# Performance work log

Measured on AMD Instinct MI355X. Metric: run time of the kernel, lower is better.

Reference implementation:

```python
import jax, jax.numpy as jnp
import numpy as np

THR = 0.5      # span-selection threshold
K_SUBJ = 16    # max subject/object spans kept per sentence (padded)
K_OBJ = 8      # max object spans kept per (subject, relation)

# Greedy threshold-based span pairing: for each start position i with
# start_prob>THR, take the first unused j>=i with end_prob>THR (NMS-like).
# Returns fixed-size padded spans [K,2] (int32) and a validity mask [K].
def greedy_spans(sp, ep, K):
    S = sp.shape[0]
    idxs = jnp.arange(S, dtype=jnp.int32)
    def step(carry, i):
        used, count, spans, valid = carry
        gate = sp[i] > THR
        cand = (ep > THR) & (~used) & (idxs >= i)
        has = jnp.any(cand)
        j = jnp.argmax(cand).astype(jnp.int32)  # first True
        found = gate & has
        slot = jnp.minimum(count, K - 1)
        write = found & (count < K)
        pair = jnp.where(write, jnp.stack([i, j]).astype(jnp.int32), spans[slot])
        spans = spans.at[slot].set(pair)
        valid = valid.at[slot].set(valid[slot] | write)
        used = used.at[j].set(used[j] | found)
        count = count + found.astype(jnp.int32)
        return (used, count, spans, valid), None
    init = (jnp.zeros(S, bool), jnp.int32(0),
            jnp.zeros((K, 2), jnp.int32), jnp.zeros(K, bool))
    (_, _, spans, valid), _ = jax.lax.scan(step, init, idxs)
    return spans, valid


def _model(token_embs, hg, rel_embs, b_rel_transe, head_w, head_b,
           Wmats, Wbias, rproj_w, rproj_b, V_w, V_b):
    # head_w/head_b order: 0 start_subj, 1 end_subj, 2 b_start_obj, 3 b_end_obj,
    #                      4 start_obj, 5 end_obj, 6 b_start_subj, 7 b_end_subj
    # Wmats/Wbias order:   0 W_s, 1 W_r, 2 W_g, 3 W_x, 4 W_r_b, 5 W_g_b, 6 W_x_b, 7 W_x2
    sig = jax.nn.sigmoid
    head = lambda x, i: sig(x @ head_w[i] + head_b[i])        # H->1 sigmoid head
    lin = lambda x, i: x @ Wmats[i].T + Wbias[i]              # H->H linear

    # ---- first-level span scores + greedy extraction (forward & backward) ----
    sub_sp, sub_ep = head(token_embs, 0), head(token_embs, 1)   # [B,S]
    bob_sp, bob_ep = head(token_embs, 2), head(token_embs, 3)
    g = jax.vmap(lambda a, b: greedy_spans(a, b, K_SUBJ))
    subj_spans, subj_valid = g(sub_sp, sub_ep)                  # [B,K,2],[B,K]
    b_subj_spans, b_subj_valid = g(bob_sp, bob_ep)

    def gather(tok_b, spans, valid):  # mean of start/end token embeddings
        e = (tok_b[spans[:, 0]] + tok_b[spans[:, 1]]) * 0.5
        return e * valid[:, None].astype(tok_b.dtype)
    s_k = jax.vmap(gather)(token_embs, subj_spans, subj_valid)      # [B,K,H]
    b_s_k = jax.vmap(gather)(token_embs, b_subj_spans, b_subj_valid)
    s_k_w = lin(s_k, 0) * subj_valid[..., None]                     # W_s + mask
    b_s_k_w = lin(b_s_k, 0) * b_subj_valid[..., None]

    # ---- relation-aware attention context C = sum_s A[b,s,r] * x[b,s] ----
    b_rel = b_rel_transe @ rproj_w.T + rproj_b                      # r_proj
    def attend(rels, ir, ig, ix):
        e = jnp.tanh(lin(token_embs, ix)[:, :, None, :]             # [B,S,1,H]
                     + lin(hg, ig)[:, None, None, :]                # [B,1,1,H]
                     + lin(rels, ir)[None, None, :, :])             # [1,1,R,H]
        v = e @ V_w + V_b[0]                                        # [B,S,R]
        A = jax.nn.softmax(v, axis=1)                               # over seq
        return jnp.einsum('bsr,bsh->brh', A, token_embs)            # [B,R,H]
    C = attend(rel_embs, 1, 2, 3)
    b_C = attend(b_rel, 4, 5, 6)

    # Heads are linear, so distribute w over the sum instead of
    # materializing the [B,S,K,R,H] tensor.
    tok_mix = token_embs + lin(token_embs, 7)
    def pair_probs(Cmat, skw, i):
        t_tok = tok_mix @ head_w[i]                                 # [B,S]
        t_sub = skw @ head_w[i]                                     # [B,K]
        t_rel = Cmat @ head_w[i]                                    # [B,R]
        return sig(t_tok[:, :, None, None] + t_sub[:, None, :, None]
                   + t_rel[:, None, None, :] + head_b[i])           # [B,S,K,R]
    obj_sp, obj_ep = pair_probs(C, s_k_w, 4), pair_probs(C, s_k_w, 5)
    bsub_sp, bsub_ep = pair_probs(b_C, b_s_k_w, 6), pair_probs(b_C, b_s_k_w, 7)

    # ---- greedy object-span extraction per (batch, subject, relation) ----
    def triples(sp4, ep4, subj_ok):
        B_, S_, K_, R_ = sp4.shape
        fsp = sp4.transpose(0, 2, 3, 1).reshape(-1, S_)
        fep = ep4.transpose(0, 2, 3, 1).reshape(-1, S_)
        spans, valid = jax.vmap(lambda a, b: greedy_spans(a, b, K_OBJ))(fsp, fep)
        spans = spans.reshape(B_, K_, R_, K_OBJ, 2)
        valid = valid.reshape(B_, K_, R_, K_OBJ) & subj_ok[:, :, None, None]
        return spans, valid
    f_spans, f_valid = triples(obj_sp, obj_ep, subj_valid)
    bw_spans, bw_valid = triples(bsub_sp, bsub_ep, b_subj_valid)

    probs = jnp.stack([obj_sp, obj_ep, bsub_sp, bsub_ep])           # [4,B,S,K,R]
    return (probs, subj_spans, subj_valid, b_subj_spans, b_subj_valid,
            f_spans, f_valid, bw_spans, bw_valid)


def setup_inputs() -> dict:
    key = jax.random.key(0)
    ks = jax.random.split(key, 12)
    B, S, H, R, T = 8, 256, 768, 40, 80
    sc = H ** -0.5
    return {
        'token_embs': jax.random.normal(ks[0], (B, S, H), jnp.float32),
        'hg': jax.random.normal(ks[1], (B, H), jnp.float32),
        'rel_embs': jax.random.normal(ks[2], (R, H), jnp.float32),
        'b_rel_transe': jax.random.normal(ks[3], (R, T), jnp.float32),
        'head_w': jax.random.normal(ks[4], (8, H), jnp.float32) * sc,
        'head_b': jax.random.normal(ks[5], (8,), jnp.float32) * 0.1,
        'Wmats': jax.random.normal(ks[6], (8, H, H), jnp.float32) * sc,
        'Wbias': jax.random.normal(ks[7], (8, H), jnp.float32) * 0.02,
        'rproj_w': jax.random.normal(ks[8], (H, T), jnp.float32) * (T ** -0.5),
        'rproj_b': jax.random.normal(ks[9], (H,), jnp.float32) * 0.02,
        'V_w': jax.random.normal(ks[10], (H,), jnp.float32) * sc,
        'V_b': jax.random.normal(ks[11], (1,), jnp.float32) * 0.1,
    }


def reference(token_embs, hg, rel_embs, b_rel_transe, head_w, head_b,
              Wmats, Wbias, rproj_w, rproj_b, V_w, V_b):
    return _model(token_embs, hg, rel_embs, b_rel_transe, head_w, head_b,
                  Wmats, Wbias, rproj_w, rproj_b, V_w, V_b)
```

## Files before the change

kernel.cpp:

```cpp
#include <hip/hip_runtime.h>
#include <hip/hip_bf16.h>
#include <stdint.h>

#define Bc 8
#define Sc 256
#define Hc 768
#define Rc 40
#define Tc 80
#define KSc 16
#define KOc 8

#define OUT_SSP 5242880
#define OUT_SVA 5243136
#define OUT_BSP 5243264
#define OUT_BVA 5243520
#define OUT_FSP 5243648
#define OUT_FVA 5325568
#define OUT_WSP 5366528
#define OUT_WVA 5448448

#define CM_PS (16 * Rc * Hc)

__device__ inline double wave_reduce_d(double v) {
#pragma unroll
  for (int o = 32; o; o >>= 1) v += __shfl_down(v, o, 64);
  return v;
}
__device__ inline float wave_reduce_f(float v) {
#pragma unroll
  for (int o = 32; o; o >>= 1) v += __shfl_down(v, o, 64);
  return v;
}

__device__ inline float tanh_fast(float x) {
  float t = __builtin_amdgcn_exp2f(x * 2.8853900817779268f);
  return fmaf(-2.f, __builtin_amdgcn_rcpf(t + 1.f), 1.f);
}

__global__ __launch_bounds__(256) void k_l03(const float* __restrict__ x,
                                             const float* __restrict__ head_w,
                                             const float* __restrict__ head_b,
                                             float* __restrict__ l03) {
  int bs = blockIdx.x * 4 + (threadIdx.x >> 6);
  int lane = threadIdx.x & 63;
  if (bs >= Bc * Sc) return;
  const float* xr = x + (size_t)bs * Hc;
  double acc[4] = {0.0, 0.0, 0.0, 0.0};
  for (int h = lane; h < Hc; h += 64) {
    double xv = (double)xr[h];
    acc[0] += xv * (double)head_w[h];
    acc[1] += xv * (double)head_w[Hc + h];
    acc[2] += xv * (double)head_w[2 * Hc + h];
    acc[3] += xv * (double)head_w[3 * Hc + h];
  }
#pragma unroll
  for (int i = 0; i < 4; ++i) {
    double a = wave_reduce_d(acc[i]);
    if (lane == 0) l03[i * (Bc * Sc) + bs] = (float)(a + (double)head_b[i]);
  }
}

__device__ inline int find_first(const uint64_t* epm, const uint64_t* used, int i) {
  int wi = i >> 6;
  uint64_t m = epm[wi] & ~used[wi] & (~0ull << (i & 63));
  if (m) return (wi << 6) + (__ffsll((unsigned long long)m) - 1);
  for (int w = wi + 1; w < 4; ++w) {
    uint64_t mm = epm[w] & ~used[w];
    if (mm) return (w << 6) + (__ffsll((unsigned long long)mm) - 1);
  }
  return -1;
}

__global__ __launch_bounds__(64) void k_greedy1(const float* __restrict__ l03,
                                                int* __restrict__ spans1, int* __restrict__ valid1,
                                                float* __restrict__ out) {
  int t = blockIdx.x;
  int dir = t >> 3, b = t & 7;
  int lane = threadIdx.x;
  const float* sp = l03 + (dir * 2) * (Bc * Sc) + b * Sc;
  const float* ep = sp + Bc * Sc;
  uint64_t spm[4], epm[4];
#pragma unroll
  for (int w = 0; w < 4; ++w) {
    spm[w] = __ballot(sp[w * 64 + lane] > 0.f);
    epm[w] = __ballot(ep[w * 64 + lane] > 0.f);
  }
  __shared__ int ssp0[KSc], ssp1[KSc], sva[KSc];
  if (lane < KSc) { ssp0[lane] = 0; ssp1[lane] = 0; sva[lane] = 0; }
  __syncthreads();
  if (lane == 0) {
    uint64_t used[4] = {0, 0, 0, 0};
    int cnt = 0;
#pragma unroll
    for (int w = 0; w < 4; ++w) {
      uint64_t g = spm[w];
      while (g) {
        int bit = __ffsll((unsigned long long)g) - 1;
        g &= g - 1;
        int i = w * 64 + bit;
        int j = find_first(epm, used, i);
        if (j < 0) continue;
        used[j >> 6] |= (1ull << (j & 63));
        if (cnt < KSc) { ssp0[cnt] = i; ssp1[cnt] = j; sva[cnt] = 1; }
        cnt++;
      }
    }
  }
  __syncthreads();
  int base = (dir * Bc + b) * KSc;
  float* osp = out + (dir ? OUT_BSP : OUT_SSP) + b * KSc * 2;
  float* ova = out + (dir ? OUT_BVA : OUT_SVA) + b * KSc;
  if (lane < KSc) {
    spans1[(base + lane) * 2] = ssp0[lane];
    spans1[(base + lane) * 2 + 1] = ssp1[lane];
    valid1[base + lane] = sva[lane];
    osp[lane * 2] = (float)ssp0[lane];
    osp[lane * 2 + 1] = (float)ssp1[lane];
    ova[lane] = (float)sva[lane];
  }
}

__global__ __launch_bounds__(256) void k_brel(const float* __restrict__ brt,
                                              const float* __restrict__ rw,
                                              const float* __restrict__ rb,
                                              float* __restrict__ brel) {
  int idx = blockIdx.x * blockDim.x + threadIdx.x;
  if (idx >= Rc * Hc) return;
  int r = idx / Hc, h = idx % Hc;
  float acc = rb[h];
  const float* a = brt + r * Tc;
  const float* w = rw + (size_t)h * Tc;
  for (int t = 0; t < Tc; ++t) acc = fmaf(a[t], w[t], acc);
  brel[idx] = acc;
}

__global__ __launch_bounds__(256) void k_egather(const float* __restrict__ x,
                                                 const int* __restrict__ spans1,
                                                 float* __restrict__ eb) {
  int row = blockIdx.x;
  int b = (row / KSc) % Bc;
  int s0 = spans1[row * 2], s1 = spans1[row * 2 + 1];
  const float* x0 = x + ((size_t)b * Sc + s0) * Hc;
  const float* x1 = x + ((size_t)b * Sc + s1) * Hc;
  float* er = eb + (size_t)row * Hc;
  for (int h = threadIdx.x; h < Hc; h += 256) er[h] = 0.5f * (x0[h] + x1[h]);
}

__global__ __launch_bounds__(256) void k_skw(const float* __restrict__ eb,
                                             const float* __restrict__ Wmats,
                                             const float* __restrict__ Wbias,
                                             const int* __restrict__ valid1,
                                             float* __restrict__ skw) {
  int m0 = blockIdx.y * 32;
  int n0 = blockIdx.x * 64;
  __shared__ float Asl[32][36];
  __shared__ float Bsl[32][68];
  int tid = threadIdx.x;
  int arow = tid >> 3, acol = (tid & 7) << 2;
  int brow = tid >> 2, bcol = (tid & 3) << 2;
  int txi = tid & 15, tyi = tid >> 4;
  const float* ap = eb + (size_t)(m0 + arow) * Hc + acol;
  const float* bp = Wmats + (size_t)(n0 + brow) * Hc + bcol;
  int nb = n0 + txi * 4;
  float4 bias = *(const float4*)&Wbias[nb];
  float acc[2][4];
#pragma unroll
  for (int i = 0; i < 2; ++i) { acc[i][0] = bias.x; acc[i][1] = bias.y; acc[i][2] = bias.z; acc[i][3] = bias.w; }
  for (int k0 = 0; k0 < Hc; k0 += 32) {
    float4 av = *(const float4*)(ap + k0);
    float4 b0 = *(const float4*)(bp + k0);
    float4 b1 = *(const float4*)(bp + k0 + 16);
    __syncthreads();
    Asl[acol + 0][arow] = av.x; Asl[acol + 1][arow] = av.y; Asl[acol + 2][arow] = av.z; Asl[acol + 3][arow] = av.w;
    Bsl[bcol + 0][brow] = b0.x; Bsl[bcol + 1][brow] = b0.y; Bsl[bcol + 2][brow] = b0.z; Bsl[bcol + 3][brow] = b0.w;
    Bsl[bcol + 16][brow] = b1.x; Bsl[bcol + 17][brow] = b1.y; Bsl[bcol + 18][brow] = b1.z; Bsl[bcol + 19][brow] = b1.w;
    __syncthreads();
#pragma unroll
    for (int kk = 0; kk < 32; ++kk) {
      float a0 = Asl[kk][tyi * 2], a1 = Asl[kk][tyi * 2 + 1];
      float4 b = *(const float4*)&Bsl[kk][txi * 4];
      acc[0][0] = fmaf(a0, b.x, acc[0][0]); acc[0][1] = fmaf(a0, b.y, acc[0][1]);
      acc[0][2] = fmaf(a0, b.z, acc[0][2]); acc[0][3] = fmaf(a0, b.w, acc[0][3]);
      acc[1][0] = fmaf(a1, b.x, acc[1][0]); acc[1][1] = fmaf(a1, b.y, acc[1][1]);
      acc[1][2] = fmaf(a1, b.z, acc[1][2]); acc[1][3] = fmaf(a1, b.w, acc[1][3]);
    }
  }
  int m_ = m0 + tyi * 2;
#pragma unroll
  for (int i = 0; i < 2; ++i) {
    int v = valid1[m_ + i];
    float4 o;
    o.x = v ? acc[i][0] : 0.f; o.y = v ? acc[i][1] : 0.f;
    o.z = v ? acc[i][2] : 0.f; o.w = v ? acc[i][3] : 0.f;
    *(float4*)&skw[(size_t)(m_ + i) * Hc + nb] = o;
  }
}

__global__ __launch_bounds__(256) void k_tgtr(const float* __restrict__ hg,
                                              const float* __restrict__ rel,
                                              const float* __restrict__ brel,
                                              const float* __restrict__ Wmats,
                                              const float* __restrict__ Wbias,
                                              float* __restrict__ tg,
                                              float* __restrict__ tr) {
  int grp = blockIdx.z;
  const float* Asrc; int M; int wsel; float* dst;
  if (grp == 0)      { Asrc = hg;   M = 8;  wsel = 2; dst = tg; }
  else if (grp == 1) { Asrc = hg;   M = 8;  wsel = 5; dst = tg + 8 * Hc; }
  else if (grp == 2) { Asrc = rel;  M = 40; wsel = 1; dst = tr; }
  else               { Asrc = brel; M = 40; wsel = 4; dst = tr + 40 * Hc; }
  int m0 = blockIdx.y * 32;
  if (m0 >= M) return;
  int n0 = blockIdx.x * 64;
  const float* W = Wmats + (size_t)wsel * Hc * Hc;
  const float* bias = Wbias + wsel * Hc;
  __shared__ float Asl[32][36];
  __shared__ float Bsl[32][68];
  int tid = threadIdx.x;
  int arow = tid >> 3, acol = (tid & 7) << 2;
  int brow = tid >> 2, bcol = (tid & 3) << 2;
  int txi = tid & 15, tyi = tid >> 4;
  int ar = m0 + arow;
  const float* ap = Asrc + (size_t)(ar < M ? ar : 0) * Hc + acol;
  const float* bp = W + (size_t)(n0 + brow) * Hc + bcol;
  int nb = n0 + txi * 4;
  float4 bv = *(const float4*)&bias[nb];
  float acc[2][4];
#pragma unroll
  for (int i = 0; i < 2; ++i) { acc[i][0] = bv.x; acc[i][1] = bv.y; acc[i][2] = bv.z; acc[i][3] = bv.w; }
  for (int k0 = 0; k0 < Hc; k0 += 32) {
    float4 av = *(const float4*)(ap + k0);
    float4 b0 = *(const float4*)(bp + k0);
    float4 b1 = *(const float4*)(bp + k0 + 16);
    __syncthreads();
    Asl[acol + 0][arow] = av.x; Asl[acol + 1][arow] = av.y; Asl[acol + 2][arow] = av.z; Asl[acol + 3][arow] = av.w;
    Bsl[bcol + 0][brow] = b0.x; Bsl[bcol + 1][brow] = b0.y; Bsl[bcol + 2][brow] = b0.z; Bsl[bcol + 3][brow] = b0.w;
    Bsl[bcol + 16][brow] = b1.x; Bsl[bcol + 17][brow] = b1.y; Bsl[bcol + 18][brow] = b1.z; Bsl[bcol + 19][brow] = b1.w;
    __syncthreads();
#pragma unroll
    for (int kk = 0; kk < 32; ++kk) {
      float a0 = Asl[kk][tyi * 2], a1 = Asl[kk][tyi * 2 + 1];
      float4 b = *(const float4*)&Bsl[kk][txi * 4];
      acc[0][0] = fmaf(a0, b.x, acc[0][0]); acc[0][1] = fmaf(a0, b.y, acc[0][1]);
      acc[0][2] = fmaf(a0, b.z, acc[0][2]); acc[0][3] = fmaf(a0, b.w, acc[0][3]);
      acc[1][0] = fmaf(a1, b.x, acc[1][0]); acc[1][1] = fmaf(a1, b.y, acc[1][1]);
      acc[1][2] = fmaf(a1, b.z, acc[1][2]); acc[1][3] = fmaf(a1, b.w, acc[1][3]);
    }
  }
  int m_ = m0 + tyi * 2;
#pragma unroll
  for (int i = 0; i < 2; ++i) {
    if (m_ + i < M) {
      float4 o; o.x = acc[i][0]; o.y = acc[i][1]; o.z = acc[i][2]; o.w = acc[i][3];
      *(float4*)&dst[(size_t)(m_ + i) * Hc + nb] = o;
    }
  }
}

#define BM 64
#define BN 64
#define BKK 32
#define LDP 68
__global__ __launch_bounds__(256) void k_tx(const float* __restrict__ x,
                                            const float* __restrict__ Wmats,
                                            const float* __restrict__ Wbias,
                                            float* __restrict__ txo) {
  int dir = blockIdx.z;
  const float* W = Wmats + (size_t)(dir ? 6 : 3) * Hc * Hc;
  const float* bias = Wbias + (dir ? 6 : 3) * Hc;
  float* outp = txo + (size_t)dir * (Bc * Sc * Hc);
  int m0 = blockIdx.y * BM;
  int n0 = blockIdx.x * BN;
  __shared__ float Asl[BKK][LDP];
  __shared__ float Bsl[BKK][LDP];
  int tid = threadIdx.x;
  int lr = tid >> 2;
  int lc = (tid & 3) << 2;
  int txi = tid & 15, tyi = tid >> 4;
  const float* xp = x + (size_t)(m0 + lr) * Hc + lc;
  const float* wp = W + (size_t)(n0 + lr) * Hc + lc;
  float4 a0 = *(const float4*)(xp);
  float4 a1 = *(const float4*)(xp + 16);
  float4 b0 = *(const float4*)(wp);
  float4 b1 = *(const float4*)(wp + 16);
  float acc[4][4] = {};
  for (int k0 = 0; k0 < Hc; k0 += BKK) {
    __syncthreads();
    Asl[lc + 0][lr] = a0.x; Asl[lc + 1][lr] = a0.y; Asl[lc + 2][lr] = a0.z; Asl[lc + 3][lr] = a0.w;
    Asl[lc + 16][lr] = a1.x; Asl[lc + 17][lr] = a1.y; Asl[lc + 18][lr] = a1.z; Asl[lc + 19][lr] = a1.w;
    Bsl[lc + 0][lr] = b0.x; Bsl[lc + 1][lr] = b0.y; Bsl[lc + 2][lr] = b0.z; Bsl[lc + 3][lr] = b0.w;
    Bsl[lc + 16][lr] = b1.x; Bsl[lc + 17][lr] = b1.y; Bsl[lc + 18][lr] = b1.z; Bsl[lc + 19][lr] = b1.w;
    __syncthreads();
    if (k0 + BKK < Hc) {
      a0 = *(const float4*)(xp + k0 + BKK);
      a1 = *(const float4*)(xp + k0 + BKK + 16);
      b0 = *(const float4*)(wp + k0 + BKK);
      b1 = *(const float4*)(wp + k0 + BKK + 16);
    }
#pragma unroll
    for (int kk = 0; kk < BKK; ++kk) {
      float4 a = *(const float4*)&Asl[kk][tyi * 4];
      float4 b = *(const float4*)&Bsl[kk][txi * 4];
      acc[0][0] = fmaf(a.x, b.x, acc[0][0]); acc[0][1] = fmaf(a.x, b.y, acc[0][1]);
      acc[0][2] = fmaf(a.x, b.z, acc[0][2]); acc[0][3] = fmaf(a.x, b.w, acc[0][3]);
      acc[1][0] = fmaf(a.y, b.x, acc[1][0]); acc[1][1] = fmaf(a.y, b.y, acc[1][1]);
      acc[1][2] = fmaf(a.y, b.z, acc[1][2]); acc[1][3] = fmaf(a.y, b.w, acc[1][3]);
      acc[2][0] = fmaf(a.z, b.x, acc[2][0]); acc[2][1] = fmaf(a.z, b.y, acc[2][1]);
      acc[2][2] = fmaf(a.z, b.z, acc[2][2]); acc[2][3] = fmaf(a.z, b.w, acc[2][3]);
      acc[3][0] = fmaf(a.w, b.x, acc[3][0]); acc[3][1] = fmaf(a.w, b.y, acc[3][1]);
      acc[3][2] = fmaf(a.w, b.z, acc[3][2]); acc[3][3] = fmaf(a.w, b.w, acc[3][3]);
    }
  }
  int nb = n0 + txi * 4;
  float4 bb = *(const float4*)&bias[nb];
#pragma unroll
  for (int i2 = 0; i2 < 4; ++i2) {
    float4 o;
    o.x = acc[i2][0] + bb.x; o.y = acc[i2][1] + bb.y;
    o.z = acc[i2][2] + bb.z; o.w = acc[i2][3] + bb.w;
    *(float4*)&outp[(size_t)(m0 + tyi * 4 + i2) * Hc + nb] = o;
  }
}

__global__ __launch_bounds__(256) void k_v(const float* __restrict__ txo,
                                           const float* __restrict__ tg,
                                           const float* __restrict__ tr,
                                           const float* __restrict__ Vw,
                                           const float* __restrict__ Vb,
                                           float* __restrict__ va) {
  int id = blockIdx.x;
  int dir = id >> 9;
  int bs0 = (id & 511) * 4;
  int b = bs0 >> 8;
  int tid = threadIdx.x;
  int wv = tid >> 6, lane = tid & 63;
  const float* tgr = tg + (dir * Bc + b) * Hc;
  float xt[4][12], vw[12];
#pragma unroll
  for (int u = 0; u < 12; ++u) {
    int h = lane + 64 * u;
    vw[u] = Vw[h];
    float tgv = tgr[h];
#pragma unroll
    for (int si = 0; si < 4; ++si)
      xt[si][u] = txo[((size_t)dir * (Bc * Sc) + bs0 + si) * Hc + h] + tgv;
  }
  float vb0 = Vb[0];
  for (int q = 0; q < 10; ++q) {
    int r = wv * 10 + q;
    const float* trr = tr + ((size_t)dir * Rc + r) * Hc + lane;
    float p0 = 0.f, p1 = 0.f, p2 = 0.f, p3 = 0.f;
#pragma unroll
    for (int u = 0; u < 12; ++u) {
      float t = trr[64 * u];
      p0 = fmaf(tanh_fast(xt[0][u] + t), vw[u], p0);
      p1 = fmaf(tanh_fast(xt[1][u] + t), vw[u], p1);
      p2 = fmaf(tanh_fast(xt[2][u] + t), vw[u], p2);
      p3 = fmaf(tanh_fast(xt[3][u] + t), vw[u], p3);
    }
    p0 = wave_reduce_f(p0); p1 = wave_reduce_f(p1);
    p2 = wave_reduce_f(p2); p3 = wave_reduce_f(p3);
    if (lane == 0) {
      size_t base = ((size_t)dir * (Bc * Sc) + bs0) * Rc + r;
      va[base] = p0 + vb0;
      va[base + Rc] = p1 + vb0;
      va[base + 2 * Rc] = p2 + vb0;
      va[base + 3 * Rc] = p3 + vb0;
    }
  }
}

__global__ __launch_bounds__(256) void k_softmax(float* __restrict__ va) {
  int id = blockIdx.x;
  int dir = id / (Bc * Rc); int rem = id % (Bc * Rc);
  int b = rem / Rc; int r = rem % Rc;
  int s = threadIdx.x;
  float* base = va + (((size_t)dir * Bc + b) * Sc) * Rc + r;
  float v = base[(size_t)s * Rc];
  __shared__ float red[8];
  float m = v;
#pragma unroll
  for (int o = 32; o; o >>= 1) m = fmaxf(m, __shfl_xor(m, o, 64));
  if ((s & 63) == 0) red[s >> 6] = m;
  __syncthreads();
  if (s == 0) red[4] = fmaxf(fmaxf(red[0], red[1]), fmaxf(red[2], red[3]));
  __syncthreads();
  m = red[4];
  float e = expf(v - m);
  float t = e;
#pragma unroll
  for (int o = 32; o; o >>= 1) t += __shfl_xor(t, o, 64);
  __syncthreads();
  if ((s & 63) == 0) red[s >> 6] = t;
  __syncthreads();
  if (s == 0) red[4] = red[0] + red[1] + red[2] + red[3];
  __syncthreads();
  base[(size_t)s * Rc] = e / red[4];
}

__global__ __launch_bounds__(256, 1) void k_C(const float* __restrict__ va,
                                              const float* __restrict__ x,
                                              float* __restrict__ Cm4) {
  int id = blockIdx.x;
  int p = id & 3;
  int g = id >> 2;
  int b = g & 7;
  __shared__ float As_[64 * Rc];
  int tid = threadIdx.x;
  const float* vab = va + ((size_t)g * Sc + p * 64) * Rc;
  for (int idx = tid; idx < 64 * Rc; idx += 256) As_[idx] = vab[idx];
  __syncthreads();
  const float* xb = x + ((size_t)b * Sc + p * 64) * Hc;
  float acc[3][Rc];
#pragma unroll
  for (int j = 0; j < 3; ++j)
#pragma unroll
    for (int r = 0; r < Rc; ++r) acc[j][r] = 0.f;
  for (int s = 0; s < 64; ++s) {
    float xv0 = xb[(size_t)s * Hc + tid];
    float xv1 = xb[(size_t)s * Hc + 256 + tid];
    float xv2 = xb[(size_t)s * Hc + 512 + tid];
#pragma unroll
    for (int q = 0; q < 10; ++q) {
      float4 a4 = *(const float4*)&As_[s * Rc + q * 4];
      acc[0][q * 4 + 0] = fmaf(a4.x, xv0, acc[0][q * 4 + 0]);
      acc[0][q * 4 + 1] = fmaf(a4.y, xv0, acc[0][q * 4 + 1]);
      acc[0][q * 4 + 2] = fmaf(a4.z, xv0, acc[0][q * 4 + 2]);
      acc[0][q * 4 + 3] = fmaf(a4.w, xv0, acc[0][q * 4 + 3]);
      acc[1][q * 4 + 0] = fmaf(a4.x, xv1, acc[1][q * 4 + 0]);
      acc[1][q * 4 + 1] = fmaf(a4.y, xv1, acc[1][q * 4 + 1]);
      acc[1][q * 4 + 2] = fmaf(a4.z, xv1, acc[1][q * 4 + 2]);
      acc[1][q * 4 + 3] = fmaf(a4.w, xv1, acc[1][q * 4 + 3]);
      acc[2][q * 4 + 0] = fmaf(a4.x, xv2, acc[2][q * 4 + 0]);
      acc[2][q * 4 + 1] = fmaf(a4.y, xv2, acc[2][q * 4 + 1]);
      acc[2][q * 4 + 2] = fmaf(a4.z, xv2, acc[2][q * 4 + 2]);
      acc[2][q * 4 + 3] = fmaf(a4.w, xv2, acc[2][q * 4 + 3]);
    }
  }
#pragma unroll
  for (int r = 0; r < Rc; ++r) {
    size_t base = ((size_t)(p * 16 + g) * Rc + r) * Hc + tid;
    Cm4[base] = acc[0][r];
    Cm4[base + 256] = acc[1][r];
    Cm4[base + 512] = acc[2][r];
  }
}

__global__ __launch_bounds__(256) void k_hv(const float* __restrict__ Wmats,
                                            const float* __restrict__ head_w,
                                            double* __restrict__ hv) {
  int idx = blockIdx.x * blockDim.x + threadIdx.x;
  if (idx >= 4 * Hc) return;
  int i = idx / Hc, j = idx % Hc;
  const float* h4 = head_w + (4 + i) * Hc;
  const float* W7 = Wmats + (size_t)7 * Hc * Hc;
  double acc = (double)h4[j];
  for (int hh = 0; hh < Hc; ++hh)
    acc += (double)W7[(size_t)hh * Hc + j] * (double)h4[hh];
  hv[idx] = acc;
}

__global__ __launch_bounds__(256) void k_tt(const float* __restrict__ x,
                                            const double* __restrict__ hv,
                                            double* __restrict__ tt) {
  int bs = blockIdx.x * 4 + (threadIdx.x >> 6);
  int lane = threadIdx.x & 63;
  if (bs >= Bc * Sc) return;
  const float* xr = x + (size_t)bs * Hc;
  double acc[4] = {0.0, 0.0, 0.0, 0.0};
  for (int h = lane; h < Hc; h += 64) {
    double xv = (double)xr[h];
    acc[0] += xv * hv[h];
    acc[1] += xv * hv[Hc + h];
    acc[2] += xv * hv[2 * Hc + h];
    acc[3] += xv * hv[3 * Hc + h];
  }
#pragma unroll
  for (int i = 0; i < 4; ++i) {
    double a = wave_reduce_d(acc[i]);
    if (lane == 0) tt[i * (Bc * Sc) + bs] = a;
  }
}

__global__ __launch_bounds__(256) void k_tsc(const float* __restrict__ skw,
                                             const float* __restrict__ Cm4,
                                             const float* __restrict__ head_w,
                                             const float* __restrict__ Wbias,
                                             double* __restrict__ ts,
                                             double* __restrict__ trl,
                                             double* __restrict__ c4) {
  int wave = blockIdx.x * 4 + (threadIdx.x >> 6);
  int lane = threadIdx.x & 63;
  const float* src; const float* w; double* dst;
  bool partial4 = false;
  if (wave < 512) {
    int p = wave >> 7, rem = wave & 127;
    int b = rem >> 4, k = rem & 15, dir = p >> 1;
    src = skw + (((size_t)(dir * Bc + b)) * KSc + k) * Hc;
    w = head_w + (4 + p) * Hc;
    dst = ts + (p * Bc + b) * KSc + k;
  } else if (wave < 1792) {
    int q = wave - 512;
    int p = q / 320, rem = q % 320;
    int b = rem / Rc, r = rem % Rc, dir = p >> 1;
    src = Cm4 + ((size_t)(dir * Bc + b) * Rc + r) * Hc;
    w = head_w + (4 + p) * Hc;
    dst = trl + (p * Bc + b) * Rc + r;
    partial4 = true;
  } else if (wave < 1796) {
    int p = wave - 1792;
    src = Wbias + 7 * Hc;
    w = head_w + (4 + p) * Hc;
    dst = c4 + p;
  } else return;
  double acc = 0.0;
  if (partial4) {
    for (int h = lane; h < Hc; h += 64) {
      double cs = (double)src[h] + (double)src[h + CM_PS] +
                  (double)src[h + 2 * CM_PS] + (double)src[h + 3 * CM_PS];
      acc += cs * (double)w[h];
    }
  } else {
    for (int h = lane; h < Hc; h += 64) acc += (double)src[h] * (double)w[h];
  }
  acc = wave_reduce_d(acc);
  if (lane == 0) *dst = acc;
}

__global__ __launch_bounds__(256) void k_probs(const double* __restrict__ tt,
                                               const double* __restrict__ ts,
                                               const double* __restrict__ trl,
                                               const double* __restrict__ c4,
                                               const float* __restrict__ head_b,
                                               float* __restrict__ out) {
  int id = blockIdx.x;
  int b = id >> 8, s = id & 255;
  (void)s;
  __shared__ double tsb[4][KSc];
  __shared__ double trb[4][Rc];
  __shared__ double basep[4];
  int tid = threadIdx.x;
  if (tid < 64) { int p = tid >> 4, k = tid & 15; tsb[p][k] = ts[(p * Bc + b) * KSc + k]; }
  if (tid < 160) { int p = tid / Rc, r = tid % Rc; trb[p][r] = trl[(p * Bc + b) * Rc + r]; }
  if (tid < 4) basep[tid] = tt[tid * (Bc * Sc) + id] + c4[tid] + (double)head_b[4 + tid];
  __syncthreads();
#pragma unroll
  for (int p = 0; p < 4; ++p) {
    double base = basep[p];
    float* op = out + ((size_t)(p * Bc) * Sc + id) * (KSc * Rc);
    for (int kr = tid; kr < KSc * Rc; kr += 256) {
      int k = kr / Rc, r = kr - k * Rc;
      double l = base + tsb[p][k] + trb[p][r];
      op[kr] = 1.f / (1.f + expf(-(float)l));
    }
  }
}

__global__ __launch_bounds__(256) void k_greedy2(const double* __restrict__ tt,
                                                 const double* __restrict__ ts,
                                                 const double* __restrict__ trl,
                                                 const double* __restrict__ c4,
                                                 const float* __restrict__ head_b,
                                                 const int* __restrict__ valid1,
                                                 float* __restrict__ out) {
  int gid = blockIdx.x * blockDim.x + threadIdx.x;
  if (gid >= 2 * Bc * KSc * Rc) return;
  int dir = gid / (Bc * KSc * Rc);
  int rem = gid % (Bc * KSc * Rc);
  int b = rem / (KSc * Rc);
  int kr = rem % (KSc * Rc);
  int k = kr / Rc, r = kr % Rc;
  int p0 = dir * 2, p1 = p0 + 1;
  double off0 = ts[(p0 * Bc + b) * KSc + k] + trl[(p0 * Bc + b) * Rc + r] + c4[p0] + (double)head_b[4 + p0];
  double off1 = ts[(p1 * Bc + b) * KSc + k] + trl[(p1 * Bc + b) * Rc + r] + c4[p1] + (double)head_b[4 + p1];
  const double* t0 = tt + p0 * (Bc * Sc) + b * Sc;
  const double* t1 = tt + p1 * (Bc * Sc) + b * Sc;
  uint64_t spm[4], epm[4], used[4] = {0, 0, 0, 0};
#pragma unroll
  for (int w = 0; w < 4; ++w) {
    uint64_t ms = 0, me = 0;
    for (int bit = 0; bit < 64; ++bit) {
      int s = w * 64 + bit;
      if (t0[s] + off0 > 0.0) ms |= (1ull << bit);
      if (t1[s] + off1 > 0.0) me |= (1ull << bit);
    }
    spm[w] = ms; epm[w] = me;
  }
  float* osp = out + (dir ? OUT_WSP : OUT_FSP) + (size_t)rem * KOc * 2;
  float* ova = out + (dir ? OUT_WVA : OUT_FVA) + (size_t)rem * KOc;
  for (int o = 0; o < KOc; ++o) { osp[o * 2] = 0.f; osp[o * 2 + 1] = 0.f; ova[o] = 0.f; }
  float sval = valid1[(dir * Bc + b) * KSc + k] ? 1.f : 0.f;
  int cnt = 0;
  for (int w = 0; w < 4; ++w) {
    uint64_t g = spm[w];
    while (g) {
      int bit = __ffsll((unsigned long long)g) - 1;
      g &= g - 1;
      int i = w * 64 + bit;
      int j = find_first(epm, used, i);
      if (j < 0) continue;
      used[j >> 6] |= (1ull << (j & 63));
      if (cnt < KOc) { osp[cnt * 2] = (float)i; osp[cnt * 2 + 1] = (float)j; ova[cnt] = sval; }
      cnt++;
    }
  }
}

extern "C" void kernel_launch(void* const* d_in, const int* in_sizes, int n_in,
                              void* d_out, int out_size, void* d_ws, size_t ws_size,
                              hipStream_t stream) {
  (void)in_sizes; (void)n_in; (void)out_size; (void)ws_size;
  const float* x = (const float*)d_in[0];
  const float* hg = (const float*)d_in[1];
  const float* rel = (const float*)d_in[2];
  const float* brt = (const float*)d_in[3];
  const float* head_w = (const float*)d_in[4];
  const float* head_b = (const float*)d_in[5];
  const float* Wmats = (const float*)d_in[6];
  const float* Wbias = (const float*)d_in[7];
  const float* rproj_w = (const float*)d_in[8];
  const float* rproj_b = (const float*)d_in[9];
  const float* Vw = (const float*)d_in[10];
  const float* Vb = (const float*)d_in[11];
  float* out = (float*)d_out;
  char* ws = (char*)d_ws;

  double* hv  = (double*)(ws + 0);
  double* c4  = (double*)(ws + 24576);
  double* tt  = (double*)(ws + 24608);
  double* ts  = (double*)(ws + 90144);
  double* trl = (double*)(ws + 94240);
  float* l03  = (float*)(ws + 104480);
  float* brel = (float*)(ws + 137248);
  float* tg   = (float*)(ws + 260128);
  float* tr   = (float*)(ws + 309280);
  float* txb  = (float*)(ws + 555040);
  float* va   = (float*)(ws + 13137952);
  float* skw  = (float*)(ws + 15759392);
  int* spans1 = (int*)(ws + 16545824);
  int* valid1 = (int*)(ws + 16547872);
  float* eb   = txb;
  float* Cm4  = txb;

  k_l03<<<512, 256, 0, stream>>>(x, head_w, head_b, l03);
  k_greedy1<<<16, 64, 0, stream>>>(l03, spans1, valid1, out);
  k_brel<<<120, 256, 0, stream>>>(brt, rproj_w, rproj_b, brel);
  k_egather<<<256, 256, 0, stream>>>(x, spans1, eb);
  k_skw<<<dim3(12, 8), 256, 0, stream>>>(eb, Wmats, Wbias, valid1, skw);
  k_tgtr<<<dim3(12, 2, 4), 256, 0, stream>>>(hg, rel, brel, Wmats, Wbias, tg, tr);
  k_tx<<<dim3(12, 32, 2), 256, 0, stream>>>(x, Wmats, Wbias, txb);
  k_v<<<1024, 256, 0, stream>>>(txb, tg, tr, Vw, Vb, va);
  k_softmax<<<640, 256, 0, stream>>>(va);
  k_C<<<64, 256, 0, stream>>>(va, x, Cm4);
  k_hv<<<12, 256, 0, stream>>>(Wmats, head_w, hv);
  k_tt<<<512, 256, 0, stream>>>(x, hv, tt);
  k_tsc<<<449, 256, 0, stream>>>(skw, Cm4, head_w, Wbias, ts, trl, c4);
  k_probs<<<2048, 256, 0, stream>>>(tt, ts, trl, c4, head_b, out);
  k_greedy2<<<40, 256, 0, stream>>>(tt, ts, trl, c4, head_b, valid1, out);
}
```

Before: 363.2 us.

## Split-K 128x128 tiled tx GEMM, merge small prep kernels into one launch

Replaces the tx projection GEMM with a split-K version that uses 128x128 tiles with 8x8 per-thread register blocking and register-prefetched shared-memory staging. Two K-halves write partial results to a new workspace buffer, and the consumer kernel sums them and adds the bias. It also merges the hv, brel and egather kernels into one launch to cut launch overhead. The split path only runs when the workspace is large enough, and it adds extra global traffic for the partial outputs.

```diff
diff --git a/kernel.cpp b/kernel.cpp
--- a/kernel.cpp
+++ b/kernel.cpp
@@ -120,30 +120,44 @@
   }
 }
 
-__global__ __launch_bounds__(256) void k_brel(const float* __restrict__ brt,
+__global__ __launch_bounds__(256) void k_prep(const float* __restrict__ brt,
                                               const float* __restrict__ rw,
                                               const float* __restrict__ rb,
-                                              float* __restrict__ brel) {
-  int idx = blockIdx.x * blockDim.x + threadIdx.x;
-  if (idx >= Rc * Hc) return;
-  int r = idx / Hc, h = idx % Hc;
-  float acc = rb[h];
-  const float* a = brt + r * Tc;
-  const float* w = rw + (size_t)h * Tc;
-  for (int t = 0; t < Tc; ++t) acc = fmaf(a[t], w[t], acc);
-  brel[idx] = acc;
-}
-
-__global__ __launch_bounds__(256) void k_egather(const float* __restrict__ x,
-                                                 const int* __restrict__ spans1,
-                                                 float* __restrict__ eb) {
-  int row = blockIdx.x;
-  int b = (row / KSc) % Bc;
-  int s0 = spans1[row * 2], s1 = spans1[row * 2 + 1];
-  const float* x0 = x + ((size_t)b * Sc + s0) * Hc;
-  const float* x1 = x + ((size_t)b * Sc + s1) * Hc;
-  float* er = eb + (size_t)row * Hc;
-  for (int h = threadIdx.x; h < Hc; h += 256) er[h] = 0.5f * (x0[h] + x1[h]);
+                                              const float* __restrict__ Wmats,
+                                              const float* __restrict__ head_w,
+                                              const float* __restrict__ x,
+                                              const int* __restrict__ spans1,
+                                              float* __restrict__ brel,
+                                              double* __restrict__ hv,
+                                              float* __restrict__ eb) {
+  int bb = blockIdx.x;
+  int tid = threadIdx.x;
+  if (bb < 12) {
+    int idx = bb * 256 + tid;
+    int i = idx / Hc, j = idx % Hc;
+    const float* h4 = head_w + (4 + i) * Hc;
+    const float* W7 = Wmats + (size_t)7 * Hc * Hc;
+    double acc = (double)h4[j];
+    for (int hh = 0; hh < Hc; ++hh)
+      acc += (double)W7[(size_t)hh * Hc + j] * (double)h4[hh];
+    hv[idx] = acc;
+  } else if (bb < 132) {
+    int idx = (bb - 12) * 256 + tid;
+    int r = idx / Hc, h = idx % Hc;
+    float acc = rb[h];
+    const float* a = brt + r * Tc;
+    const float* w = rw + (size_t)h * Tc;
+    for (int t = 0; t < Tc; ++t) acc = fmaf(a[t], w[t], acc);
+    brel[idx] = acc;
+  } else {
+    int row = bb - 132;
+    int b = (row / KSc) % Bc;
+    int s0 = spans1[row * 2], s1 = spans1[row * 2 + 1];
+    const float* x0 = x + ((size_t)b * Sc + s0) * Hc;
+    const float* x1 = x + ((size_t)b * Sc + s1) * Hc;
+    float* er = eb + (size_t)row * Hc;
+    for (int h = tid; h < Hc; h += 256) er[h] = 0.5f * (x0[h] + x1[h]);
+  }
 }
 
 __global__ __launch_bounds__(256) void k_skw(const float* __restrict__ eb,
@@ -322,6 +336,72 @@
   }
 }
 
+__global__ __launch_bounds__(256) void k_tx2(const float* __restrict__ x,
+                                             const float* __restrict__ Wmats,
+                                             float* __restrict__ txp) {
+  int z = blockIdx.z;
+  int dir = z >> 1, half = z & 1;
+  const float* W = Wmats + (size_t)(dir ? 6 : 3) * Hc * Hc;
+  float* outp = txp + (size_t)z * (Bc * Sc * Hc);
+  int m0 = blockIdx.y * 128;
+  int n0 = blockIdx.x * 128;
+  int kb = half * 384;
+  __shared__ float Asl[16 * 132];
+  __shared__ float Bsl[16 * 132];
+  int tid = threadIdx.x;
+  int txi = tid & 15, tyi = tid >> 4;
+  int sr = tid >> 1, skq = (tid & 1) * 8;
+  const float* xp = x + (size_t)(m0 + sr) * Hc + kb + skq;
+  const float* wp = W + (size_t)(n0 + sr) * Hc + kb + skq;
+  float* aw = &Asl[(sr >> 3) * 132 + (sr & 7)];
+  float* bw = &Bsl[(sr >> 3) * 132 + (sr & 7)];
+  const float* arp = &Asl[tyi * 132];
+  const float* brp = &Bsl[txi * 132];
+  float4 a0 = *(const float4*)(xp);
+  float4 a1 = *(const float4*)(xp + 4);
+  float4 b0 = *(const float4*)(wp);
+  float4 b1 = *(const float4*)(wp + 4);
+  float acc[8][8] = {};
+  for (int kt = 0; kt < 24; ++kt) {
+    __syncthreads();
+    aw[(skq + 0) * 8] = a0.x; aw[(skq + 1) * 8] = a0.y; aw[(skq + 2) * 8] = a0.z; aw[(skq + 3) * 8] = a0.w;
+    aw[(skq + 4) * 8] = a1.x; aw[(skq + 5) * 8] = a1.y; aw[(skq + 6) * 8] = a1.z; aw[(skq + 7) * 8] = a1.w;
+    bw[(skq + 0) * 8] = b0.x; bw[(skq + 1) * 8] = b0.y; bw[(skq + 2) * 8] = b0.z; bw[(skq + 3) * 8] = b0.w;
+    bw[(skq + 4) * 8] = b1.x; bw[(skq + 5) * 8] = b1.y; bw[(skq + 6) * 8] = b1.z; bw[(skq + 7) * 8] = b1.w;
+    __syncthreads();
+    if (kt + 1 < 24) {
+      int ko = (kt + 1) * 16;
+      a0 = *(const float4*)(xp + ko);
+      a1 = *(const float4*)(xp + ko + 4);
+      b0 = *(const float4*)(wp + ko);
+      b1 = *(const float4*)(wp + ko + 4);
+    }
+#pragma unroll
+    for (int kk = 0; kk < 16; ++kk) {
+      float4 A0 = *(const float4*)&arp[kk * 8];
+      float4 A1 = *(const float4*)&arp[kk * 8 + 4];
+      float4 B0 = *(const float4*)&brp[kk * 8];
+      float4 B1 = *(const float4*)&brp[kk * 8 + 4];
+      float aF[8] = {A0.x, A0.y, A0.z, A0.w, A1.x, A1.y, A1.z, A1.w};
+      float bF[8] = {B0.x, B0.y, B0.z, B0.w, B1.x, B1.y, B1.z, B1.w};
+#pragma unroll
+      for (int i = 0; i < 8; ++i)
+#pragma unroll
+        for (int j = 0; j < 8; ++j)
+          acc[i][j] = fmaf(aF[i], bF[j], acc[i][j]);
+    }
+  }
+#pragma unroll
+  for (int i = 0; i < 8; ++i) {
+    float* orow = outp + (size_t)(m0 + tyi * 8 + i) * Hc + n0 + txi * 8;
+    float4 o0, o1;
+    o0.x = acc[i][0]; o0.y = acc[i][1]; o0.z = acc[i][2]; o0.w = acc[i][3];
+    o1.x = acc[i][4]; o1.y = acc[i][5]; o1.z = acc[i][6]; o1.w = acc[i][7];
+    *(float4*)orow = o0;
+    *(float4*)(orow + 4) = o1;
+  }
+}
+
 __global__ __launch_bounds__(256) void k_v(const float* __restrict__ txo,
                                            const float* __restrict__ tg,
                                            const float* __restrict__ tr,
@@ -344,6 +424,60 @@
 #pragma unroll
     for (int si = 0; si < 4; ++si)
       xt[si][u] = txo[((size_t)dir * (Bc * Sc) + bs0 + si) * Hc + h] + tgv;
+  }
+  float vb0 = Vb[0];
+  for (int q = 0; q < 10; ++q) {
+    int r = wv * 10 + q;
+    const float* trr = tr + ((size_t)dir * Rc + r) * Hc + lane;
+    float p0 = 0.f, p1 = 0.f, p2 = 0.f, p3 = 0.f;
+#pragma unroll
+    for (int u = 0; u < 12; ++u) {
+      float t = trr[64 * u];
+      p0 = fmaf(tanh_fast(xt[0][u] + t), vw[u], p0);
+      p1 = fmaf(tanh_fast(xt[1][u] + t), vw[u], p1);
+      p2 = fmaf(tanh_fast(xt[2][u] + t), vw[u], p2);
+      p3 = fmaf(tanh_fast(xt[3][u] + t), vw[u], p3);
+    }
+    p0 = wave_reduce_f(p0); p1 = wave_reduce_f(p1);
+    p2 = wave_reduce_f(p2); p3 = wave_reduce_f(p3);
+    if (lane == 0) {
+      size_t base = ((size_t)dir * (Bc * Sc) + bs0) * Rc + r;
+      va[base] = p0 + vb0;
+      va[base + Rc] = p1 + vb0;
+      va[base + 2 * Rc] = p2 + vb0;
+      va[base + 3 * Rc] = p3 + vb0;
+    }
+  }
+}
+
+__global__ __launch_bounds__(256) void k_v2(const float* __restrict__ txp,
+                                            const float* __restrict__ Wbias,
+                                            const float* __restrict__ tg,
+                                            const float* __restrict__ tr,
+                                            const float* __restrict__ Vw,
+                                            const float* __restrict__ Vb,
+                                            float* __restrict__ va) {
+  int id = blockIdx.x;
+  int dir = id >> 9;
+  int bs0 = (id & 511) * 4;
+  int b = bs0 >> 8;
+  int tid = threadIdx.x;
+  int wv = tid >> 6, lane = tid & 63;
+  const float* tgr = tg + (dir * Bc + b) * Hc;
+  const float* wb = Wbias + (dir ? 6 : 3) * Hc;
+  const float* p0p = txp + (size_t)(dir * 2) * (Bc * Sc) * Hc;
+  const float* p1p = p0p + (size_t)(Bc * Sc) * Hc;
+  float xt[4][12], vw[12];
+#pragma unroll
+  for (int u = 0; u < 12; ++u) {
+    int h = lane + 64 * u;
+    vw[u] = Vw[h];
+    float cv = wb[h] + tgr[h];
+#pragma unroll
+    for (int si = 0; si < 4; ++si) {
+      size_t idx = (size_t)(bs0 + si) * Hc + h;
+      xt[si][u] = (p0p[idx] + p1p[idx]) + cv;
+    }
   }
   float vb0 = Vb[0];
   for (int q = 0; q < 10; ++q) {
@@ -444,20 +578,6 @@
     Cm4[base + 256] = acc[1][r];
     Cm4[base + 512] = acc[2][r];
   }
-}
-
-__global__ __launch_bounds__(256) void k_hv(const float* __restrict__ Wmats,
-                                            const float* __restrict__ head_w,
-                                            double* __restrict__ hv) {
-  int idx = blockIdx.x * blockDim.x + threadIdx.x;
-  if (idx >= 4 * Hc) return;
-  int i = idx / Hc, j = idx % Hc;
-  const float* h4 = head_w + (4 + i) * Hc;
-  const float* W7 = Wmats + (size_t)7 * Hc * Hc;
-  double acc = (double)h4[j];
-  for (int hh = 0; hh < Hc; ++hh)
-    acc += (double)W7[(size_t)hh * Hc + j] * (double)h4[hh];
-  hv[idx] = acc;
 }
 
 __global__ __launch_bounds__(256) void k_tt(const float* __restrict__ x,
@@ -609,7 +729,7 @@
 extern "C" void kernel_launch(void* const* d_in, const int* in_sizes, int n_in,
                               void* d_out, int out_size, void* d_ws, size_t ws_size,
                               hipStream_t stream) {
-  (void)in_sizes; (void)n_in; (void)out_size; (void)ws_size;
+  (void)in_sizes; (void)n_in; (void)out_size;
   const float* x = (const float*)d_in[0];
   const float* hg = (const float*)d_in[1];
   const float* rel = (const float*)d_in[2];
@@ -641,18 +761,23 @@
   int* valid1 = (int*)(ws + 16547872);
   float* eb   = txb;
   float* Cm4  = txb;
+  float* txp  = (float*)(ws + 16549376);
+  const bool split = ws_size >= (size_t)16549376 + (size_t)4 * Bc * Sc * Hc * 4;
 
   k_l03<<<512, 256, 0, stream>>>(x, head_w, head_b, l03);
   k_greedy1<<<16, 64, 0, stream>>>(l03, spans1, valid1, out);
-  k_brel<<<120, 256, 0, stream>>>(brt, rproj_w, rproj_b, brel);
-  k_egather<<<256, 256, 0, stream>>>(x, spans1, eb);
+  k_prep<<<388, 256, 0, stream>>>(brt, rproj_w, rproj_b, Wmats, head_w, x, spans1, brel, hv, eb);
   k_skw<<<dim3(12, 8), 256, 0, stream>>>(eb, Wmats, Wbias, valid1, skw);
   k_tgtr<<<dim3(12, 2, 4), 256, 0, stream>>>(hg, rel, brel, Wmats, Wbias, tg, tr);
-  k_tx<<<dim3(12, 32, 2), 256, 0, stream>>>(x, Wmats, Wbias, txb);
-  k_v<<<1024, 256, 0, stream>>>(txb, tg, tr, Vw, Vb, va);
+  if (split) {
+    k_tx2<<<dim3(6, 16, 4), 256, 0, stream>>>(x, Wmats, txp);
+    k_v2<<<1024, 256, 0, stream>>>(txp, Wbias, tg, tr, Vw, Vb, va);
+  } else {
+    k_tx<<<dim3(12, 32, 2), 256, 0, stream>>>(x, Wmats, Wbias, txb);
+    k_v<<<1024, 256, 0, stream>>>(txb, tg, tr, Vw, Vb, va);
+  }
   k_softmax<<<640, 256, 0, stream>>>(va);
   k_C<<<64, 256, 0, stream>>>(va, x, Cm4);
-  k_hv<<<12, 256, 0, stream>>>(Wmats, head_w, hv);
   k_tt<<<512, 256, 0, stream>>>(x, hv, tt);
   k_tsc<<<449, 256, 0, stream>>>(skw, Cm4, head_w, Wbias, ts, trl, c4);
   k_probs<<<2048, 256, 0, stream>>>(tt, ts, trl, c4, head_b, out);
```

After: 360.6 us. No clear change (-0.7%).

## Merge prep kernels into one launch, split k_v over relation halves, prescale tanh

Applied to the files above, without the earlier changes.

Fuses k_brel, k_egather and k_hv into a single k_prep kernel that branches on block index, which saves two launches and lets the serial double-precision hv work overlap with the other small jobs. k_v now launches twice as many blocks, each covering half the relations, to raise parallelism. It also folds the tanh exp2 scale constant into the preloaded activations and into each t, which drops a multiply from the inner loop. The trade-off is that each k_v block reloads its x/tg rows, doubling that traffic, and hv is now computed earlier in the stream than before.

```diff
diff --git a/kernel.cpp b/kernel.cpp
--- a/kernel.cpp
+++ b/kernel.cpp
@@ -20,6 +20,7 @@
 #define OUT_WVA 5448448
 
 #define CM_PS (16 * Rc * Hc)
+#define BSH (Bc * Sc * Hc)
 
 __device__ inline double wave_reduce_d(double v) {
 #pragma unroll
@@ -30,11 +31,6 @@
 #pragma unroll
   for (int o = 32; o; o >>= 1) v += __shfl_down(v, o, 64);
   return v;
-}
-
-__device__ inline float tanh_fast(float x) {
-  float t = __builtin_amdgcn_exp2f(x * 2.8853900817779268f);
-  return fmaf(-2.f, __builtin_amdgcn_rcpf(t + 1.f), 1.f);
 }
 
 __global__ __launch_bounds__(256) void k_l03(const float* __restrict__ x,
@@ -120,30 +116,44 @@
   }
 }
 
-__global__ __launch_bounds__(256) void k_brel(const float* __restrict__ brt,
+__global__ __launch_bounds__(256) void k_prep(const float* __restrict__ brt,
                                               const float* __restrict__ rw,
                                               const float* __restrict__ rb,
-                                              float* __restrict__ brel) {
-  int idx = blockIdx.x * blockDim.x + threadIdx.x;
-  if (idx >= Rc * Hc) return;
-  int r = idx / Hc, h = idx % Hc;
-  float acc = rb[h];
-  const float* a = brt + r * Tc;
-  const float* w = rw + (size_t)h * Tc;
-  for (int t = 0; t < Tc; ++t) acc = fmaf(a[t], w[t], acc);
-  brel[idx] = acc;
-}
-
-__global__ __launch_bounds__(256) void k_egather(const float* __restrict__ x,
-                                                 const int* __restrict__ spans1,
-                                                 float* __restrict__ eb) {
-  int row = blockIdx.x;
-  int b = (row / KSc) % Bc;
-  int s0 = spans1[row * 2], s1 = spans1[row * 2 + 1];
-  const float* x0 = x + ((size_t)b * Sc + s0) * Hc;
-  const float* x1 = x + ((size_t)b * Sc + s1) * Hc;
-  float* er = eb + (size_t)row * Hc;
-  for (int h = threadIdx.x; h < Hc; h += 256) er[h] = 0.5f * (x0[h] + x1[h]);
+                                              const float* __restrict__ Wmats,
+                                              const float* __restrict__ head_w,
+                                              const float* __restrict__ x,
+                                              const int* __restrict__ spans1,
+                                              float* __restrict__ brel,
+                                              double* __restrict__ hv,
+                                              float* __restrict__ eb) {
+  int bb = blockIdx.x;
+  int tid = threadIdx.x;
+  if (bb < 12) {
+    int idx = bb * 256 + tid;
+    int i = idx / Hc, j = idx % Hc;
+    const float* h4 = head_w + (4 + i) * Hc;
+    const float* W7 = Wmats + (size_t)7 * Hc * Hc;
+    double acc = (double)h4[j];
+    for (int hh = 0; hh < Hc; ++hh)
+      acc += (double)W7[(size_t)hh * Hc + j] * (double)h4[hh];
+    hv[idx] = acc;
+  } else if (bb < 132) {
+    int idx = (bb - 12) * 256 + tid;
+    int r = idx / Hc, h = idx % Hc;
+    float acc = rb[h];
+    const float* a = brt + r * Tc;
+    const float* w = rw + (size_t)h * Tc;
+    for (int t = 0; t < Tc; ++t) acc = fmaf(a[t], w[t], acc);
+    brel[idx] = acc;
+  } else {
+    int row = bb - 132;
+    int b = (row / KSc) % Bc;
+    int s0 = spans1[row * 2], s1 = spans1[row * 2 + 1];
+    const float* x0 = x + ((size_t)b * Sc + s0) * Hc;
+    const float* x1 = x + ((size_t)b * Sc + s1) * Hc;
+    float* er = eb + (size_t)row * Hc;
+    for (int h = tid; h < Hc; h += 256) er[h] = 0.5f * (x0[h] + x1[h]);
+  }
 }
 
 __global__ __launch_bounds__(256) void k_skw(const float* __restrict__ eb,
@@ -268,7 +278,7 @@
   int dir = blockIdx.z;
   const float* W = Wmats + (size_t)(dir ? 6 : 3) * Hc * Hc;
   const float* bias = Wbias + (dir ? 6 : 3) * Hc;
-  float* outp = txo + (size_t)dir * (Bc * Sc * Hc);
+  float* outp = txo + (size_t)dir * BSH;
   int m0 = blockIdx.y * BM;
   int n0 = blockIdx.x * BN;
   __shared__ float Asl[BKK][LDP];
@@ -328,9 +338,12 @@
                                            const float* __restrict__ Vw,
                                            const float* __restrict__ Vb,
                                            float* __restrict__ va) {
+  const float Cl = 2.8853900817779268f;
   int id = blockIdx.x;
-  int dir = id >> 9;
-  int bs0 = (id & 511) * 4;
+  int dir = id >> 10;
+  int rem = id & 1023;
+  int rhalf = rem & 1;
+  int bs0 = (rem >> 1) * 4;
   int b = bs0 >> 8;
   int tid = threadIdx.x;
   int wv = tid >> 6, lane = tid & 63;
@@ -343,20 +356,24 @@
     float tgv = tgr[h];
 #pragma unroll
     for (int si = 0; si < 4; ++si)
-      xt[si][u] = txo[((size_t)dir * (Bc * Sc) + bs0 + si) * Hc + h] + tgv;
+      xt[si][u] = (txo[((size_t)dir * (Bc * Sc) + bs0 + si) * Hc + h] + tgv) * Cl;
   }
   float vb0 = Vb[0];
-  for (int q = 0; q < 10; ++q) {
-    int r = wv * 10 + q;
+  for (int q = 0; q < 5; ++q) {
+    int r = rhalf * 20 + wv * 5 + q;
     const float* trr = tr + ((size_t)dir * Rc + r) * Hc + lane;
     float p0 = 0.f, p1 = 0.f, p2 = 0.f, p3 = 0.f;
 #pragma unroll
     for (int u = 0; u < 12; ++u) {
-      float t = trr[64 * u];
-      p0 = fmaf(tanh_fast(xt[0][u] + t), vw[u], p0);
-      p1 = fmaf(tanh_fast(xt[1][u] + t), vw[u], p1);
-      p2 = fmaf(tanh_fast(xt[2][u] + t), vw[u], p2);
-      p3 = fmaf(tanh_fast(xt[3][u] + t), vw[u], p3);
+      float t = trr[64 * u] * Cl;
+      float e0 = __builtin_amdgcn_exp2f(xt[0][u] + t);
+      float e1 = __builtin_amdgcn_exp2f(xt[1][u] + t);
+      float e2 = __builtin_amdgcn_exp2f(xt[2][u] + t);
+      float e3 = __builtin_amdgcn_exp2f(xt[3][u] + t);
+      p0 = fmaf(fmaf(-2.f, __builtin_amdgcn_rcpf(e0 + 1.f), 1.f), vw[u], p0);
+      p1 = fmaf(fmaf(-2.f, __builtin_amdgcn_rcpf(e1 + 1.f), 1.f), vw[u], p1);
+      p2 = fmaf(fmaf(-2.f, __builtin_amdgcn_rcpf(e2 + 1.f), 1.f), vw[u], p2);
+      p3 = fmaf(fmaf(-2.f, __builtin_amdgcn_rcpf(e3 + 1.f), 1.f), vw[u], p3);
     }
     p0 = wave_reduce_f(p0); p1 = wave_reduce_f(p1);
     p2 = wave_reduce_f(p2); p3 = wave_reduce_f(p3);
@@ -444,20 +461,6 @@
     Cm4[base + 256] = acc[1][r];
     Cm4[base + 512] = acc[2][r];
   }
-}
-
-__global__ __launch_bounds__(256) void k_hv(const float* __restrict__ Wmats,
-                                            const float* __restrict__ head_w,
-                                            double* __restrict__ hv) {
-  int idx = blockIdx.x * blockDim.x + threadIdx.x;
-  if (idx >= 4 * Hc) return;
-  int i = idx / Hc, j = idx % Hc;
-  const float* h4 = head_w + (4 + i) * Hc;
-  const float* W7 = Wmats + (size_t)7 * Hc * Hc;
-  double acc = (double)h4[j];
-  for (int hh = 0; hh < Hc; ++hh)
-    acc += (double)W7[(size_t)hh * Hc + j] * (double)h4[hh];
-  hv[idx] = acc;
 }
 
 __global__ __launch_bounds__(256) void k_tt(const float* __restrict__ x,
@@ -644,15 +647,13 @@
 
   k_l03<<<512, 256, 0, stream>>>(x, head_w, head_b, l03);
   k_greedy1<<<16, 64, 0, stream>>>(l03, spans1, valid1, out);
-  k_brel<<<120, 256, 0, stream>>>(brt, rproj_w, rproj_b, brel);
-  k_egather<<<256, 256, 0, stream>>>(x, spans1, eb);
+  k_prep<<<388, 256, 0, stream>>>(brt, rproj_w, rproj_b, Wmats, head_w, x, spans1, brel, hv, eb);
   k_skw<<<dim3(12, 8), 256, 0, stream>>>(eb, Wmats, Wbias, valid1, skw);
   k_tgtr<<<dim3(12, 2, 4), 256, 0, stream>>>(hg, rel, brel, Wmats, Wbias, tg, tr);
   k_tx<<<dim3(12, 32, 2), 256, 0, stream>>>(x, Wmats, Wbias, txb);
-  k_v<<<1024, 256, 0, stream>>>(txb, tg, tr, Vw, Vb, va);
+  k_v<<<2048, 256, 0, stream>>>(txb, tg, tr, Vw, Vb, va);
   k_softmax<<<640, 256, 0, stream>>>(va);
   k_C<<<64, 256, 0, stream>>>(va, x, Cm4);
-  k_hv<<<12, 256, 0, stream>>>(Wmats, head_w, hv);
   k_tt<<<512, 256, 0, stream>>>(x, hv, tt);
   k_tsc<<<449, 256, 0, stream>>>(skw, Cm4, head_w, Wbias, ts, trl, c4);
   k_probs<<<2048, 256, 0, stream>>>(tt, ts, trl, c4, head_b, out);
```

Result: faster. 353.2 us (-2.7%).
